# Kernel tuning notes

Hardware: AMD Instinct MI355X
Metric: run time of the kernel (lower is better)

The kernel has to match this reference:

```python
import jax, jax.numpy as jnp
import numpy as np

NUM_STREAM = 4
SINKHORN_ITERS = 20
HC_EPS = 1e-06
NORM_EPS = 1e-06


def sinkhorn_knopps(h, iters, eps):
    # h: [B, S, ns, ns]
    h = jax.nn.softmax(h, axis=-1) + eps
    h = h / (h.sum(-2, keepdims=True) + eps)
    for _ in range(iters - 1):  # fixed small trip count (19), unrolled
        h = h / (h.sum(-1, keepdims=True) + eps)
        h = h / (h.sum(-2, keepdims=True) + eps)
    return h


def setup_inputs() -> dict:
    key = jax.random.key(0)
    k1, k2, k3, k4 = jax.random.split(key, 4)
    B, S, ns, H = 4, 2048, NUM_STREAM, 1024
    mix_hc = (2 + ns) * ns  # 24
    x = jax.random.normal(k1, (B, S, ns, H), dtype=jnp.float32)
    hc_fn = jax.random.normal(k2, (mix_hc, ns * H), dtype=jnp.float32) * 0.02
    hc_scale = jax.random.uniform(k3, (3,), dtype=jnp.float32)
    hc_base = jax.random.normal(k4, (mix_hc,), dtype=jnp.float32)
    return {"x": x, "hc_fn": hc_fn, "hc_scale": hc_scale, "hc_base": hc_base}


def reference(x, hc_fn, hc_scale, hc_base):
    B, S, ns, H = x.shape
    xf = x.reshape(B, S, ns * H).astype(jnp.float32)
    # RMSNorm stats (applied as a post-scale on the linear output, as in source)
    rsqrt = jax.lax.rsqrt(jnp.mean(jnp.square(xf), axis=-1, keepdims=True) + NORM_EPS)
    weight = jnp.einsum('bsd,md->bsm', xf, hc_fn) * rsqrt  # [B, S, mix_hc]
    h_pre = weight[..., :ns]
    h_post = weight[..., ns:2 * ns]
    h_res = weight[..., 2 * ns:].reshape(B, S, ns, ns)
    h_pre = jax.nn.sigmoid(h_pre * hc_scale[0] + hc_base[:ns][None, None, :]) + HC_EPS
    h_post = 2.0 * jax.nn.sigmoid(h_post * hc_scale[1] + hc_base[ns:2 * ns][None, None, :])
    h_res = h_res * hc_scale[2] + hc_base[2 * ns:].reshape(ns, ns)[None, None, :, :]
    h_res = sinkhorn_knopps(h_res, SINKHORN_ITERS, HC_EPS)
    xs = xf.reshape(B, S, ns, H)
    # hc_pre: mix streams into a single vector per token
    y = jnp.einsum('bsn,bsnh->bsh', h_pre, xs)  # [B, S, H]
    # hc_post: broadcast gated y back to streams + Sinkhorn-mixed residual streams
    out = h_post[..., None] * y[:, :, None, :] + jnp.einsum('bsij,bsih->bsjh', h_res, xs)
    return out.astype(x.dtype)
```

## Files before the change

### kernel.cpp

```cpp
#include <hip/hip_runtime.h>
#include <math.h>

#define NS 4
#define HDIM 1024
#define DDIM 4096
#define TOK_B 8
#define KCH 256
#define NCH 16
#define HC_EPS_F 1e-6f
#define NORM_EPS_F 1e-6f

typedef __attribute__((ext_vector_type(8))) short short8;
typedef __attribute__((ext_vector_type(4))) float f32x4;

__device__ __forceinline__ float frcp(float v) { return __builtin_amdgcn_rcpf(v); }

__device__ __forceinline__ void gload_lds16(const float* g, float* l) {
  __builtin_amdgcn_global_load_lds(
      (const __attribute__((address_space(1))) void*)g,
      (__attribute__((address_space(3))) void*)l, 16, 0, 0);
}

#define CVT_PAIR(j, f0, f1)                                                     \
  { unsigned p0 = __float_as_uint(f0), p1 = __float_as_uint(f1);                \
    H.u[j] = (p1 & 0xFFFF0000u) | (p0 >> 16);                                   \
    unsigned q0 = __float_as_uint((f0) - __uint_as_float(p0 & 0xFFFF0000u));    \
    unsigned q1 = __float_as_uint((f1) - __uint_as_float(p1 & 0xFFFF0000u));    \
    L.u[j] = (q1 & 0xFFFF0000u) | (q0 >> 16); }

__device__ __forceinline__ void cvt_hl(const float4 a, const float4 b,
                                       short8& hi, short8& lo) {
  union { unsigned u[4]; short8 s; } H, L;
  CVT_PAIR(0, a.x, a.y)
  CVT_PAIR(1, a.z, a.w)
  CVT_PAIR(2, b.x, b.y)
  CVT_PAIR(3, b.z, b.w)
  hi = H.s; lo = L.s;
}

__launch_bounds__(256, 4)
__global__ void mhc_convb(const float* __restrict__ hc_fn,
                          unsigned short* __restrict__ bh,
                          unsigned short* __restrict__ bl) {
  const int g = blockIdx.x * 256 + threadIdx.x;
  const float4 v = ((const float4*)hc_fn)[g];
  ushort4 h, l;
  unsigned p;
  p = __float_as_uint(v.x); h.x = p >> 16; l.x = __float_as_uint(v.x - __uint_as_float(p & 0xFFFF0000u)) >> 16;
  p = __float_as_uint(v.y); h.y = p >> 16; l.y = __float_as_uint(v.y - __uint_as_float(p & 0xFFFF0000u)) >> 16;
  p = __float_as_uint(v.z); h.z = p >> 16; l.z = __float_as_uint(v.z - __uint_as_float(p & 0xFFFF0000u)) >> 16;
  p = __float_as_uint(v.w); h.w = p >> 16; l.w = __float_as_uint(v.w - __uint_as_float(p & 0xFFFF0000u)) >> 16;
  ((ushort4*)bh)[g] = h;
  ((ushort4*)bl)[g] = l;
}

__launch_bounds__(256, 2)
__global__ void mhc_fused(const float* __restrict__ x,
                          const unsigned short* __restrict__ bh,
                          const unsigned short* __restrict__ bl,
                          const float* __restrict__ hc_scale,
                          const float* __restrict__ hc_base,
                          float* __restrict__ gates, int ntok) {
  __shared__ float xs[2][TOK_B * KCH];
  __shared__ float wsl[4][TOK_B][25];
  const int tid  = threadIdx.x;
  const int lane = tid & 63;
  const int wave = tid >> 6;
  const long long tok0 = (long long)blockIdx.x * TOK_B;

#define STAGE(d, kcn)                                                           \
  {                                                                             \
    _Pragma("unroll")                                                           \
    for (int c = 0; c < 2; ++c) {                                               \
      const int S = c * 256 + wave * 64;                  \
      const int t = S >> 6;                                 \
      const int c4src = lane ^ (t & 7);                                         \
      gload_lds16(x + (tok0 + t) * DDIM + (kcn) * KCH + c4src * 4,              \
                  &xs[d][(size_t)S * 4]);                                       \
    }                                                                           \
  }

  const int kh   = wave;
  const int row  = lane & 15;
  const int trow = row & 7;
  const int ks   = lane >> 4;

  const unsigned short* bp0h = bh + (long long)row * DDIM + kh * 64 + ks * 8;
  const unsigned short* bp0l = bl + (long long)row * DDIM + kh * 64 + ks * 8;
  const int fr1c = (row < 8) ? (16 + row) : 23;
  const unsigned short* bp1h = bh + (long long)fr1c * DDIM + kh * 64 + ks * 8;
  const unsigned short* bp1l = bl + (long long)fr1c * DDIM + kh * 64 + ks * 8;
  const bool v1 = (row < 8);
  const short8 z8 = {0, 0, 0, 0, 0, 0, 0, 0};

  f32x4 acc0 = {0.f, 0.f, 0.f, 0.f};
  f32x4 acc1 = {0.f, 0.f, 0.f, 0.f};
  float ssq = 0.f;

  STAGE(0, 0)
  __syncthreads();

  const float* arow0 = xs[0] + (size_t)trow * KCH;
  const float* arow1 = xs[1] + (size_t)trow * KCH;

  for (int kc = 0; kc < NCH; ++kc) {
    if (kc < NCH - 1) {
      if (kc & 1) STAGE(0, kc + 1) else STAGE(1, kc + 1)
    }
    const float* arow = (kc & 1) ? arow1 : arow0;

    #pragma unroll
    for (int s = 0; s < 2; ++s) {
      const int ko = kc * KCH + s * 32;
      const short8 b0h = *(const short8*)(bp0h + ko);
      const short8 b0l = *(const short8*)(bp0l + ko);
      const short8 b1h = v1 ? *(const short8*)(bp1h + ko) : z8;
      const short8 b1l = v1 ? *(const short8*)(bp1l + ko) : z8;

      const int c4 = kh * 16 + s * 8 + ks * 2;
      const float4 a0 = *(const float4*)(arow + (size_t)((c4) ^ trow) * 4);
      const float4 a1 = *(const float4*)(arow + (size_t)((c4 + 1) ^ trow) * 4);

      ssq = fmaf(a0.x, a0.x, fmaf(a0.y, a0.y, fmaf(a0.z, a0.z, fmaf(a0.w, a0.w, ssq))));
      ssq = fmaf(a1.x, a1.x, fmaf(a1.y, a1.y, fmaf(a1.z, a1.z, fmaf(a1.w, a1.w, ssq))));

      short8 ahi, alo;
      cvt_hl(a0, a1, ahi, alo);

      acc0 = __builtin_amdgcn_mfma_f32_16x16x32_bf16(ahi, b0h, acc0, 0, 0, 0);
      acc1 = __builtin_amdgcn_mfma_f32_16x16x32_bf16(ahi, b1h, acc1, 0, 0, 0);
      acc0 = __builtin_amdgcn_mfma_f32_16x16x32_bf16(ahi, b0l, acc0, 0, 0, 0);
      acc1 = __builtin_amdgcn_mfma_f32_16x16x32_bf16(ahi, b1l, acc1, 0, 0, 0);
      acc0 = __builtin_amdgcn_mfma_f32_16x16x32_bf16(alo, b0h, acc0, 0, 0, 0);
      acc1 = __builtin_amdgcn_mfma_f32_16x16x32_bf16(alo, b1h, acc1, 0, 0, 0);
    }
    __syncthreads();
  }
#undef STAGE

  const int rq = lane >> 4;
  if (rq < 2) {
    #pragma unroll
    for (int r = 0; r < 4; ++r) wsl[kh][rq * 4 + r][row] = acc0[r];
    if (row < 8) {
      #pragma unroll
      for (int r = 0; r < 4; ++r) wsl[kh][rq * 4 + r][16 + row] = acc1[r];
    }
  }
  ssq += __shfl_xor(ssq, 16, 64);
  ssq += __shfl_xor(ssq, 32, 64);
  if (ks == 0 && row < 8) wsl[kh][row][24] = ssq;
  __syncthreads();

  if (wave < 2) {
    const int tt = wave * 4 + (lane >> 4);
    const int e  = lane & 15;
    float sres = wsl[0][tt][8 + e] + wsl[1][tt][8 + e] + wsl[2][tt][8 + e] + wsl[3][tt][8 + e];
    float ssqt = wsl[0][tt][24] + wsl[1][tt][24] + wsl[2][tt][24] + wsl[3][tt][24];
    float spre = 0.f, spost = 0.f;
    if (e < NS) {
      spre  = wsl[0][tt][e] + wsl[1][tt][e] + wsl[2][tt][e] + wsl[3][tt][e];
      spost = wsl[0][tt][NS + e] + wsl[1][tt][NS + e] + wsl[2][tt][NS + e] + wsl[3][tt][NS + e];
    }

    const float rs = rsqrtf(ssqt * (1.0f / DDIM) + NORM_EPS_F);
    const float s0 = hc_scale[0], s1 = hc_scale[1], s2 = hc_scale[2];

    float h = sres * rs * s2 + hc_base[8 + e];
    float mx = fmaxf(h, __shfl_xor(h, 1, 4));
    mx = fmaxf(mx, __shfl_xor(mx, 2, 4));
    float ex = expf(h - mx);
    float sm = ex + __shfl_xor(ex, 1, 4);
    sm += __shfl_xor(sm, 2, 4);
    h = ex * frcp(sm) + HC_EPS_F;
    float cs = h + __shfl_xor(h, 4, 16);
    cs += __shfl_xor(cs, 8, 16);
    h *= frcp(cs + HC_EPS_F);
    #pragma unroll 1
    for (int itn = 0; itn < 19; ++itn) {
      float rsum = h + __shfl_xor(h, 1, 4);
      rsum += __shfl_xor(rsum, 2, 4);
      h *= frcp(rsum + HC_EPS_F);
      float csum = h + __shfl_xor(h, 4, 16);
      csum += __shfl_xor(csum, 8, 16);
      h *= frcp(csum + HC_EPS_F);
    }
    gates[(size_t)(8 + e) * ntok + tok0 + tt] = h;
    if (e < NS) {
      gates[(size_t)e * ntok + tok0 + tt] =
          frcp(1.0f + expf(-(spre * rs * s0 + hc_base[e]))) + HC_EPS_F;
      gates[(size_t)(NS + e) * ntok + tok0 + tt] =
          2.0f * frcp(1.0f + expf(-(spost * rs * s1 + hc_base[NS + e])));
    }
  }
}

__launch_bounds__(256, 8)
__global__ void mhc_out(const float* __restrict__ x,
                        const float* __restrict__ gates,
                        float* __restrict__ out, int ntok) {
  const long long token = blockIdx.x;
  const int q = threadIdx.x;

  float hp[NS], hq[NS], hr[NS][NS];
  #pragma unroll
  for (int i = 0; i < NS; ++i) {
    hp[i] = gates[(size_t)i * ntok + token];
    hq[i] = gates[(size_t)(NS + i) * ntok + token];
    #pragma unroll
    for (int j = 0; j < NS; ++j)
      hr[i][j] = gates[(size_t)(8 + i * NS + j) * ntok + token];
  }

  const float4* xb = (const float4*)(x + token * DDIM);
  float4 xv[NS];
  #pragma unroll
  for (int i = 0; i < NS; ++i) xv[i] = xb[i * 256 + q];

  float4 y;
  y.x = hp[0]*xv[0].x + hp[1]*xv[1].x + hp[2]*xv[2].x + hp[3]*xv[3].x;
  y.y = hp[0]*xv[0].y + hp[1]*xv[1].y + hp[2]*xv[2].y + hp[3]*xv[3].y;
  y.z = hp[0]*xv[0].z + hp[1]*xv[1].z + hp[2]*xv[2].z + hp[3]*xv[3].z;
  y.w = hp[0]*xv[0].w + hp[1]*xv[1].w + hp[2]*xv[2].w + hp[3]*xv[3].w;

  float4* ob = (float4*)(out + token * DDIM);
  #pragma unroll
  for (int n = 0; n < NS; ++n) {
    float4 o;
    o.x = hq[n]*y.x + hr[0][n]*xv[0].x + hr[1][n]*xv[1].x + hr[2][n]*xv[2].x + hr[3][n]*xv[3].x;
    o.y = hq[n]*y.y + hr[0][n]*xv[0].y + hr[1][n]*xv[1].y + hr[2][n]*xv[2].y + hr[3][n]*xv[3].y;
    o.z = hq[n]*y.z + hr[0][n]*xv[0].z + hr[1][n]*xv[1].z + hr[2][n]*xv[2].z + hr[3][n]*xv[3].z;
    o.w = hq[n]*y.w + hr[0][n]*xv[0].w + hr[1][n]*xv[1].w + hr[2][n]*xv[2].w + hr[3][n]*xv[3].w;
    ob[n * 256 + q] = o;
  }
}

extern "C" void kernel_launch(void* const* d_in, const int* in_sizes, int n_in,
                              void* d_out, int out_size, void* d_ws, size_t ws_size,
                              hipStream_t stream) {
  const float* x        = (const float*)d_in[0];
  const float* hc_fn    = (const float*)d_in[1];
  const float* hc_scale = (const float*)d_in[2];
  const float* hc_base  = (const float*)d_in[3];
  float* out = (float*)d_out;

  const int ntok = in_sizes[0] / DDIM;
  float* gates = (float*)d_ws;

  unsigned short* bh = (unsigned short*)out;
  unsigned short* bl = bh + 24 * DDIM;

  mhc_convb<<<(24 * DDIM / 4) / 256, 256, 0, stream>>>(hc_fn, bh, bl);
  mhc_fused<<<ntok / TOK_B, 256, 0, stream>>>(x, bh, bl, hc_scale, hc_base, gates, ntok);
  mhc_out<<<ntok, 256, 0, stream>>>(x, gates, out, ntok);
}
```

Before: 111.1 us.

## Deepen LDS staging to four buffers and prefetch B fragments a chunk ahead

```diff
diff --git a/kernel.cpp b/kernel.cpp
--- a/kernel.cpp
+++ b/kernel.cpp
@@ -7,6 +7,7 @@
 #define TOK_B 8
 #define KCH 256
 #define NCH 16
+#define NBUF 4
 #define HC_EPS_F 1e-6f
 #define NORM_EPS_F 1e-6f
 
@@ -61,7 +62,7 @@
                           const float* __restrict__ hc_scale,
                           const float* __restrict__ hc_base,
                           float* __restrict__ gates, int ntok) {
-  __shared__ float xs[2][TOK_B * KCH];
+  __shared__ float xs[NBUF][TOK_B * KCH];
   __shared__ float wsl[4][TOK_B][25];
   const int tid  = threadIdx.x;
   const int lane = tid & 63;
@@ -74,7 +75,7 @@
     for (int c = 0; c < 2; ++c) {                                               \
       const int S = c * 256 + wave * 64;                  \
       const int t = S >> 6;                                 \
-      const int c4src = lane ^ (t & 7);                                         \
+      const int c4src = lane ^ t;                                               \
       gload_lds16(x + (tok0 + t) * DDIM + (kcn) * KCH + c4src * 4,              \
                   &xs[d][(size_t)S * 4]);                                       \
     }                                                                           \
@@ -97,45 +98,74 @@
   f32x4 acc1 = {0.f, 0.f, 0.f, 0.f};
   float ssq = 0.f;
 
+  short8 BA0h, BA0l, BA1h, BA1l, BA2h, BA2l, BA3h, BA3l;
+  short8 BB0h, BB0l, BB1h, BB1l, BB2h, BB2l, BB3h, BB3l;
+
+#define LOADB(P, kcn)                                                           \
+  P##0h = *(const short8*)(bp0h + (kcn) * KCH);                                 \
+  P##0l = *(const short8*)(bp0l + (kcn) * KCH);                                 \
+  P##1h = v1 ? *(const short8*)(bp1h + (kcn) * KCH) : z8;                       \
+  P##1l = v1 ? *(const short8*)(bp1l + (kcn) * KCH) : z8;                       \
+  P##2h = *(const short8*)(bp0h + (kcn) * KCH + 32);                            \
+  P##2l = *(const short8*)(bp0l + (kcn) * KCH + 32);                            \
+  P##3h = v1 ? *(const short8*)(bp1h + (kcn) * KCH + 32) : z8;                  \
+  P##3l = v1 ? *(const short8*)(bp1l + (kcn) * KCH + 32) : z8;
+
+#define KSTEP(arow, s, BH0, BL0, BH1, BL1)                                      \
+  {                                                                             \
+    const int c4 = kh * 16 + (s) * 8 + ks * 2;                                  \
+    const float4 a0 = *(const float4*)((arow) + (size_t)((c4) ^ trow) * 4);     \
+    const float4 a1 = *(const float4*)((arow) + (size_t)((c4 + 1) ^ trow) * 4); \
+    ssq = fmaf(a0.x, a0.x, fmaf(a0.y, a0.y, fmaf(a0.z, a0.z, fmaf(a0.w, a0.w, ssq)))); \
+    ssq = fmaf(a1.x, a1.x, fmaf(a1.y, a1.y, fmaf(a1.z, a1.z, fmaf(a1.w, a1.w, ssq)))); \
+    short8 ahi, alo;                                                            \
+    cvt_hl(a0, a1, ahi, alo);                                                   \
+    acc0 = __builtin_amdgcn_mfma_f32_16x16x32_bf16(ahi, BH0, acc0, 0, 0, 0);    \
+    acc1 = __builtin_amdgcn_mfma_f32_16x16x32_bf16(ahi, BH1, acc1, 0, 0, 0);    \
+    acc0 = __builtin_amdgcn_mfma_f32_16x16x32_bf16(ahi, BL0, acc0, 0, 0, 0);    \
+    acc1 = __builtin_amdgcn_mfma_f32_16x16x32_bf16(ahi, BL1, acc1, 0, 0, 0);    \
+    acc0 = __builtin_amdgcn_mfma_f32_16x16x32_bf16(alo, BH0, acc0, 0, 0, 0);    \
+    acc1 = __builtin_amdgcn_mfma_f32_16x16x32_bf16(alo, BH1, acc1, 0, 0, 0);    \
+  }
+
+#define ITER(kc, SC, SN, VM, DO_B, DO_S)                                        \
+  {                                                                             \
+    asm volatile("s_waitcnt vmcnt(" #VM ")" ::: "memory");                      \
+    __builtin_amdgcn_sched_barrier(0);                                          \
+    __builtin_amdgcn_s_barrier();                                               \
+    __builtin_amdgcn_sched_barrier(0);                                          \
+    const float* arow = xs[(kc) & 3] + (size_t)trow * KCH;                      \
+    KSTEP(arow, 0, SC##0h, SC##0l, SC##1h, SC##1l)                              \
+    KSTEP(arow, 1, SC##2h, SC##2l, SC##3h, SC##3l)                              \
+    if (DO_B) { LOADB(SN, (kc) + 1) }                                           \
+    if (DO_S) STAGE(((kc) + 3) & 3, (kc) + 3)                                   \
+  }
+
   STAGE(0, 0)
-  __syncthreads();
-
-  const float* arow0 = xs[0] + (size_t)trow * KCH;
-  const float* arow1 = xs[1] + (size_t)trow * KCH;
-
-  for (int kc = 0; kc < NCH; ++kc) {
-    if (kc < NCH - 1) {
-      if (kc & 1) STAGE(0, kc + 1) else STAGE(1, kc + 1)
-    }
-    const float* arow = (kc & 1) ? arow1 : arow0;
-
-    #pragma unroll
-    for (int s = 0; s < 2; ++s) {
-      const int ko = kc * KCH + s * 32;
-      const short8 b0h = *(const short8*)(bp0h + ko);
-      const short8 b0l = *(const short8*)(bp0l + ko);
-      const short8 b1h = v1 ? *(const short8*)(bp1h + ko) : z8;
-      const short8 b1l = v1 ? *(const short8*)(bp1l + ko) : z8;
-
-      const int c4 = kh * 16 + s * 8 + ks * 2;
-      const float4 a0 = *(const float4*)(arow + (size_t)((c4) ^ trow) * 4);
-      const float4 a1 = *(const float4*)(arow + (size_t)((c4 + 1) ^ trow) * 4);
-
-      ssq = fmaf(a0.x, a0.x, fmaf(a0.y, a0.y, fmaf(a0.z, a0.z, fmaf(a0.w, a0.w, ssq))));
-      ssq = fmaf(a1.x, a1.x, fmaf(a1.y, a1.y, fmaf(a1.z, a1.z, fmaf(a1.w, a1.w, ssq))));
-
-      short8 ahi, alo;
-      cvt_hl(a0, a1, ahi, alo);
-
-      acc0 = __builtin_amdgcn_mfma_f32_16x16x32_bf16(ahi, b0h, acc0, 0, 0, 0);
-      acc1 = __builtin_amdgcn_mfma_f32_16x16x32_bf16(ahi, b1h, acc1, 0, 0, 0);
-      acc0 = __builtin_amdgcn_mfma_f32_16x16x32_bf16(ahi, b0l, acc0, 0, 0, 0);
-      acc1 = __builtin_amdgcn_mfma_f32_16x16x32_bf16(ahi, b1l, acc1, 0, 0, 0);
-      acc0 = __builtin_amdgcn_mfma_f32_16x16x32_bf16(alo, b0h, acc0, 0, 0, 0);
-      acc1 = __builtin_amdgcn_mfma_f32_16x16x32_bf16(alo, b1h, acc1, 0, 0, 0);
-    }
-    __syncthreads();
-  }
+  STAGE(1, 1)
+  LOADB(BA, 0)
+  STAGE(2, 2)
+
+  ITER(0,  BA, BB, 2, 1, 1)
+  ITER(1,  BB, BA, 2, 1, 1)
+  ITER(2,  BA, BB, 2, 1, 1)
+  ITER(3,  BB, BA, 2, 1, 1)
+  ITER(4,  BA, BB, 2, 1, 1)
+  ITER(5,  BB, BA, 2, 1, 1)
+  ITER(6,  BA, BB, 2, 1, 1)
+  ITER(7,  BB, BA, 2, 1, 1)
+  ITER(8,  BA, BB, 2, 1, 1)
+  ITER(9,  BB, BA, 2, 1, 1)
+  ITER(10, BA, BB, 2, 1, 1)
+  ITER(11, BB, BA, 2, 1, 1)
+  ITER(12, BA, BB, 2, 1, 1)
+  ITER(13, BB, BA, 2, 1, 0)
+  ITER(14, BA, BB, 0, 1, 0)
+  ITER(15, BB, BA, 0, 0, 0)
+
+#undef ITER
+#undef KSTEP
+#undef LOADB
 #undef STAGE
 
   const int rq = lane >> 4;
```

Result: slower. 134.1 us (+20.7%).
